# Kernel tuning notes

Hardware: AMD Instinct MI355X
Metric: run time of the kernel (lower is better)

## Reference

```python
import jax, jax.numpy as jnp
import numpy as np

SCALE = 8.0  # sqrt(hid=64), passed as init arg `scale`


def setup_inputs() -> dict:
    key = jax.random.key(0)
    kq, kk, kv, km = jax.random.split(key, 4)
    B, S, H = 32, 2048, 64  # B = bs*n_head
    q = jax.random.normal(kq, (B, S, H), dtype=jnp.float32)
    k = jax.random.normal(kk, (B, S, H), dtype=jnp.float32)
    v = jax.random.normal(kv, (B, S, H), dtype=jnp.float32)
    mask = jax.random.bernoulli(km, 0.1, (B, S, S))  # True = masked out
    return {"q": q, "k": k, "v": v, "mask": mask, "cca": 0}


def reference(q, k, v, mask, cca):
    # scores: [B, Sq, Sk]
    attn = jnp.einsum('bqh,bkh->bqk', q, k) / SCALE
    if mask is not None:
        attn = jnp.where(mask, jnp.finfo(q.dtype).min, attn)
    if cca:
        # CCA branch: softmax over the query/sequence axis (dim=1)
        attn = jax.nn.softmax(attn, axis=1)
        ctx = jnp.einsum('bq,bkh->bqh', attn.squeeze(-1)[..., None].squeeze(-1), v) if attn.ndim == 2 else jnp.einsum('bqk,bkh->bqh', attn, v)
    else:
        attn = jax.nn.softmax(attn, axis=2)
        ctx = jnp.einsum('bqk,bkh->bqh', attn, v)  # [B, Sq, H]
    return (ctx, attn)
```

## Files before the change

### kernel.cpp

```cpp
#include <hip/hip_runtime.h>
#include <hip/hip_bf16.h>

typedef __bf16  bf16x8_t __attribute__((ext_vector_type(8)));
typedef float   f32x4_t  __attribute__((ext_vector_type(4)));
typedef short   s16x8_t  __attribute__((ext_vector_type(8)));

#define S_LEN    2048
#define HDIM     64
#define BQ       16
#define NTHREADS 512
#define PSTR     2056
#define QSTR     72

__device__ __forceinline__ short f2bf(float f) {
    return __builtin_bit_cast(short, (__bf16)f);
}
__device__ __forceinline__ float bf2f(short s) {
    return __builtin_bit_cast(float, ((unsigned)(unsigned short)s) << 16);
}

__global__ void detect_mask(const unsigned char* __restrict__ M, int* __restrict__ flags) {
    __shared__ int cnt[4];
    if (threadIdx.x < 4) cnt[threadIdx.x] = 0;
    __syncthreads();
    int local[4] = {0, 0, 0, 0};
    for (int i = threadIdx.x; i < 16384; i += 256)
        if (M[i]) local[i & 3]++;
    #pragma unroll
    for (int c = 0; c < 4; ++c)
        if (local[c]) atomicAdd(&cnt[c], local[c]);
    __syncthreads();
    if (threadIdx.x == 0) {
        int stride;
        if (cnt[1] == 0 && cnt[2] == 0 && cnt[3] == 0)      stride = 4;
        else if (cnt[0] == 0 && cnt[1] == 0)                stride = 4;
        else                                                stride = 1;
        flags[0] = stride;
    }
}

__global__ __launch_bounds__(NTHREADS, 4)
void sdpa_fused(const float* __restrict__ Q, const float* __restrict__ K,
                const float* __restrict__ V, const unsigned char* __restrict__ M,
                const int* __restrict__ MF, float* __restrict__ OUT)
{
    __shared__ short Plds[BQ * PSTR];
    __shared__ short Qlds[BQ * QSTR];
    __shared__ float rowsum[BQ];

    const int tid  = threadIdx.x;
    const int wave = tid >> 6;
    const int lane = tid & 63;
    const int col  = lane & 15;
    const int kg   = lane >> 4;

    const int mstride = MF[0];

    const int id   = blockIdx.x;
    const int slot = id >> 3;
    const int b    = ((slot >> 7) << 3) | (id & 7);
    const int q0   = (slot & 127) * BQ;

    float* ctx_out  = OUT;
    float* attn_out = OUT + (size_t)32 * S_LEN * HDIM;

    {
        const int r  = tid >> 5;
        const int h2 = (tid & 31) * 2;
        const float2 qv = *(const float2*)(Q + ((size_t)b * S_LEN + q0 + r) * HDIM + h2);
        Qlds[r * QSTR + h2]     = f2bf(qv.x);
        Qlds[r * QSTR + h2 + 1] = f2bf(qv.y);
    }
    __syncthreads();

    bf16x8_t afrag[2];
    #pragma unroll
    for (int kk = 0; kk < 2; ++kk)
        afrag[kk] = *(const bf16x8_t*)&Qlds[col * QSTR + kk * 32 + kg * 8];

    {
        const float* Kb = K + (size_t)b * S_LEN * HDIM;
        #pragma unroll 2
        for (int f = 0; f < 16; ++f) {
            const int n0 = wave * 256 + f * 16;
            const float* kp = Kb + (n0 + col) * HDIM + kg * 8;
            const float4 ka = *(const float4*)kp;
            const float4 kb = *(const float4*)(kp + 4);
            const float4 kc = *(const float4*)(kp + 32);
            const float4 kd = *(const float4*)(kp + 36);
            s16x8_t b0s, b1s;
            b0s[0]=f2bf(ka.x); b0s[1]=f2bf(ka.y); b0s[2]=f2bf(ka.z); b0s[3]=f2bf(ka.w);
            b0s[4]=f2bf(kb.x); b0s[5]=f2bf(kb.y); b0s[6]=f2bf(kb.z); b0s[7]=f2bf(kb.w);
            b1s[0]=f2bf(kc.x); b1s[1]=f2bf(kc.y); b1s[2]=f2bf(kc.z); b1s[3]=f2bf(kc.w);
            b1s[4]=f2bf(kd.x); b1s[5]=f2bf(kd.y); b1s[6]=f2bf(kd.z); b1s[7]=f2bf(kd.w);
            f32x4_t acc = {0.f, 0.f, 0.f, 0.f};
            acc = __builtin_amdgcn_mfma_f32_16x16x32_bf16(afrag[0], __builtin_bit_cast(bf16x8_t, b0s), acc, 0, 0, 0);
            acc = __builtin_amdgcn_mfma_f32_16x16x32_bf16(afrag[1], __builtin_bit_cast(bf16x8_t, b1s), acc, 0, 0, 0);
            #pragma unroll
            for (int r = 0; r < 4; ++r)
                Plds[(kg*4 + r) * PSTR + n0 + col] = f2bf(__expf(acc[r] * 0.125f));
        }
    }
    __syncthreads();

    {
        const int row = tid >> 5;
        const int lr  = tid & 31;
        float s = 0.f;
        if (mstride == 1) {
            const unsigned char* mrow = M + (size_t)b * S_LEN * S_LEN + (size_t)(q0 + row) * S_LEN;
            #pragma unroll 2
            for (int i = 0; i < 8; ++i) {
                const int c0 = (lr + 32 * i) * 8;
                s16x8_t pv = *(s16x8_t*)&Plds[row * PSTR + c0];
                const uint2 mm = *(const uint2*)(mrow + c0);
                #pragma unroll
                for (int e = 0; e < 4; ++e) {
                    if ((mm.x >> (8*e)) & 0xFFu) pv[e] = 0; else s += bf2f(pv[e]);
                    if ((mm.y >> (8*e)) & 0xFFu) pv[4+e] = 0; else s += bf2f(pv[4+e]);
                }
                *(s16x8_t*)&Plds[row * PSTR + c0] = pv;
            }
        } else {
            const unsigned* mrow = (const unsigned*)M + (size_t)b * S_LEN * S_LEN + (size_t)(q0 + row) * S_LEN;
            #pragma unroll 2
            for (int i = 0; i < 8; ++i) {
                const int c0 = (lr + 32 * i) * 8;
                s16x8_t pv = *(s16x8_t*)&Plds[row * PSTR + c0];
                const uint4 w0 = *(const uint4*)(mrow + c0);
                const uint4 w1 = *(const uint4*)(mrow + c0 + 4);
                if (w0.x) pv[0] = 0; else s += bf2f(pv[0]);
                if (w0.y) pv[1] = 0; else s += bf2f(pv[1]);
                if (w0.z) pv[2] = 0; else s += bf2f(pv[2]);
                if (w0.w) pv[3] = 0; else s += bf2f(pv[3]);
                if (w1.x) pv[4] = 0; else s += bf2f(pv[4]);
                if (w1.y) pv[5] = 0; else s += bf2f(pv[5]);
                if (w1.z) pv[6] = 0; else s += bf2f(pv[6]);
                if (w1.w) pv[7] = 0; else s += bf2f(pv[7]);
                *(s16x8_t*)&Plds[row * PSTR + c0] = pv;
            }
        }
        s += __shfl_xor(s, 1);
        s += __shfl_xor(s, 2);
        s += __shfl_xor(s, 4);
        s += __shfl_xor(s, 8);
        s += __shfl_xor(s, 16);
        if (lr == 0) rowsum[row] = s;
    }
    __syncthreads();

    if (wave < 4) {
        float* ab = attn_out + ((size_t)b * S_LEN + q0) * S_LEN;
        #pragma unroll 2
        for (int it = 0; it < 16; ++it) {
            const int flat = it * 256 + tid;
            const int row  = flat >> 8;
            const int c0   = (flat & 255) * 8;
            const float inv = 1.0f / rowsum[row];
            const s16x8_t pv = *(const s16x8_t*)&Plds[row * PSTR + c0];
            float4 o0, o1;
            o0.x = bf2f(pv[0]) * inv; o0.y = bf2f(pv[1]) * inv;
            o0.z = bf2f(pv[2]) * inv; o0.w = bf2f(pv[3]) * inv;
            o1.x = bf2f(pv[4]) * inv; o1.y = bf2f(pv[5]) * inv;
            o1.z = bf2f(pv[6]) * inv; o1.w = bf2f(pv[7]) * inv;
            float* op = ab + (size_t)row * S_LEN + c0;
            *(float4*)op       = o0;
            *(float4*)(op + 4) = o1;
        }
    } else {
        const int hbase = (wave - 4) * 16;
        const float* Vb = V + (size_t)b * S_LEN * HDIM + hbase + col;

        float p0[8], p1[8];
        #define LOADV(k0, dst)                                          \
            { const float* vp = Vb + (size_t)((k0) + kg * 8) * HDIM;    \
              dst[0] = vp[0*HDIM]; dst[1] = vp[1*HDIM];                 \
              dst[2] = vp[2*HDIM]; dst[3] = vp[3*HDIM];                 \
              dst[4] = vp[4*HDIM]; dst[5] = vp[5*HDIM];                 \
              dst[6] = vp[6*HDIM]; dst[7] = vp[7*HDIM]; }
        #define PACK(src, dst)                                          \
            { s16x8_t t;                                                \
              t[0]=f2bf(src[0]); t[1]=f2bf(src[1]); t[2]=f2bf(src[2]);  \
              t[3]=f2bf(src[3]); t[4]=f2bf(src[4]); t[5]=f2bf(src[5]);  \
              t[6]=f2bf(src[6]); t[7]=f2bf(src[7]);                     \
              dst = __builtin_bit_cast(bf16x8_t, t); }

        LOADV(0,  p0);
        LOADV(32, p1);
        f32x4_t cacc = {0.f, 0.f, 0.f, 0.f};
        for (int kc2 = 0; kc2 < 32; ++kc2) {
            const int ke = kc2 * 2;
            {
                const bf16x8_t pa = *(const bf16x8_t*)&Plds[col * PSTR + ke*32 + kg*8];
                bf16x8_t vbf; PACK(p0, vbf);
                if (ke + 2 < 64) LOADV((ke + 2) * 32, p0);
                cacc = __builtin_amdgcn_mfma_f32_16x16x32_bf16(pa, vbf, cacc, 0, 0, 0);
            }
            {
                const bf16x8_t pa = *(const bf16x8_t*)&Plds[col * PSTR + (ke+1)*32 + kg*8];
                bf16x8_t vbf; PACK(p1, vbf);
                if (ke + 3 < 64) LOADV((ke + 3) * 32, p1);
                cacc = __builtin_amdgcn_mfma_f32_16x16x32_bf16(pa, vbf, cacc, 0, 0, 0);
            }
        }
        #undef LOADV
        #undef PACK
        #pragma unroll
        for (int r = 0; r < 4; ++r) {
            const int row = kg * 4 + r;
            ctx_out[((size_t)b * S_LEN + q0 + row) * HDIM + hbase + col] = cacc[r] / rowsum[row];
        }
    }
}

extern "C" void kernel_launch(void* const* d_in, const int* in_sizes, int n_in,
                              void* d_out, int out_size, void* d_ws, size_t ws_size,
                              hipStream_t stream)
{
    const float* q = (const float*)d_in[0];
    const float* k = (const float*)d_in[1];
    const float* v = (const float*)d_in[2];
    const unsigned char* mask = (const unsigned char*)d_in[3];
    int* mflags = (int*)d_ws;
    float* out = (float*)d_out;
    detect_mask<<<dim3(1), dim3(256), 0, stream>>>(mask, mflags);
    sdpa_fused<<<dim3(4096), dim3(NTHREADS), 0, stream>>>(q, k, v, mask, mflags, out);
}
```

Before: 508.2 us.

## Prefetch mask as bitmask, fuse masking into QK, split PV across all waves

The mask row block is loaded up front with nontemporal loads and compressed into a per-row bitmask in shared memory. Masking and row-sum accumulation are then folded into the QK^T/exp loop, which removes a separate pass over P and a barrier. The PV product is split across all eight waves by key halves, with a shared-memory reduction, and all waves now cooperate on the attention store using nontemporal stores. Extra shared memory (bitmask, partials) and more registers from the unrolled K prefetch could lower occupancy.

```diff
diff --git a/kernel.cpp b/kernel.cpp
--- a/kernel.cpp
+++ b/kernel.cpp
@@ -1,9 +1,10 @@
 #include <hip/hip_runtime.h>
 #include <hip/hip_bf16.h>
 
-typedef __bf16  bf16x8_t __attribute__((ext_vector_type(8)));
-typedef float   f32x4_t  __attribute__((ext_vector_type(4)));
-typedef short   s16x8_t  __attribute__((ext_vector_type(8)));
+typedef __bf16    bf16x8_t __attribute__((ext_vector_type(8)));
+typedef float     f32x4_t  __attribute__((ext_vector_type(4)));
+typedef short     s16x8_t  __attribute__((ext_vector_type(8)));
+typedef unsigned  u32x4_t  __attribute__((ext_vector_type(4)));
 
 #define S_LEN    2048
 #define HDIM     64
@@ -11,6 +12,7 @@
 #define NTHREADS 512
 #define PSTR     2056
 #define QSTR     72
+#define BMSTR    264
 
 __device__ __forceinline__ short f2bf(float f) {
     return __builtin_bit_cast(short, (__bf16)f);
@@ -46,14 +48,16 @@
 {
     __shared__ short Plds[BQ * PSTR];
     __shared__ short Qlds[BQ * QSTR];
+    __shared__ unsigned char Bm[BQ * BMSTR];
+    __shared__ float Pvp[4][BQ][17];
     __shared__ float rowsum[BQ];
+    __shared__ float rinv[BQ];
 
     const int tid  = threadIdx.x;
     const int wave = tid >> 6;
     const int lane = tid & 63;
     const int col  = lane & 15;
     const int kg   = lane >> 4;
-
     const int mstride = MF[0];
 
     const int id   = blockIdx.x;
@@ -70,6 +74,46 @@
         const float2 qv = *(const float2*)(Q + ((size_t)b * S_LEN + q0 + r) * HDIM + h2);
         Qlds[r * QSTR + h2]     = f2bf(qv.x);
         Qlds[r * QSTR + h2 + 1] = f2bf(qv.y);
+        if (tid < BQ) rowsum[tid] = 0.f;
+    }
+    {
+        const int row = tid >> 5;
+        const int seg = (tid & 31) * 64;
+        unsigned nib[16];
+        if (mstride == 1) {
+            const unsigned char* mp = M + (size_t)b * S_LEN * S_LEN
+                                        + (size_t)(q0 + row) * S_LEN + seg;
+            const u32x4_t m0 = __builtin_nontemporal_load((const u32x4_t*)(mp));
+            const u32x4_t m1 = __builtin_nontemporal_load((const u32x4_t*)(mp + 16));
+            const u32x4_t m2 = __builtin_nontemporal_load((const u32x4_t*)(mp + 32));
+            const u32x4_t m3 = __builtin_nontemporal_load((const u32x4_t*)(mp + 48));
+            const unsigned w[16] = {m0[0],m0[1],m0[2],m0[3], m1[0],m1[1],m1[2],m1[3],
+                                    m2[0],m2[1],m2[2],m2[3], m3[0],m3[1],m3[2],m3[3]};
+            #pragma unroll
+            for (int i = 0; i < 16; ++i) {
+                const unsigned t = (w[i] & 0x7F7F7F7Fu) + 0x7F7F7F7Fu;
+                const unsigned z = ((t | w[i]) & 0x80808080u) >> 7;
+                nib[i] = (z * 0x10204081u) >> 28;
+            }
+        } else {
+            const unsigned* mp = (const unsigned*)M + (size_t)b * S_LEN * S_LEN
+                                    + (size_t)(q0 + row) * S_LEN + seg;
+            #pragma unroll
+            for (int j = 0; j < 16; ++j) {
+                const u32x4_t wv = __builtin_nontemporal_load((const u32x4_t*)(mp + j * 4));
+                unsigned n = 0, t;
+                t = (wv[0] & 0x7FFFFFFFu) + 0x7FFFFFFFu; n |=  ((t | wv[0]) >> 31) & 1u;
+                t = (wv[1] & 0x7FFFFFFFu) + 0x7FFFFFFFu; n |= (((t | wv[1]) >> 31) & 1u) << 1;
+                t = (wv[2] & 0x7FFFFFFFu) + 0x7FFFFFFFu; n |= (((t | wv[2]) >> 31) & 1u) << 2;
+                t = (wv[3] & 0x7FFFFFFFu) + 0x7FFFFFFFu; n |= (((t | wv[3]) >> 31) & 1u) << 3;
+                nib[j] = n;
+            }
+        }
+        unsigned lo = 0, hi = 0;
+        #pragma unroll
+        for (int j = 0; j < 8; ++j) { lo |= nib[j] << (4 * j); hi |= nib[8 + j] << (4 * j); }
+        *(unsigned long long*)&Bm[row * BMSTR + (seg >> 3)] =
+            ((unsigned long long)hi << 32) | lo;
     }
     __syncthreads();
 
@@ -78,137 +122,126 @@
     for (int kk = 0; kk < 2; ++kk)
         afrag[kk] = *(const bf16x8_t*)&Qlds[col * QSTR + kk * 32 + kg * 8];
 
+    float rs[4] = {0.f, 0.f, 0.f, 0.f};
     {
         const float* Kb = K + (size_t)b * S_LEN * HDIM;
-        #pragma unroll 2
-        for (int f = 0; f < 16; ++f) {
-            const int n0 = wave * 256 + f * 16;
-            const float* kp = Kb + (n0 + col) * HDIM + kg * 8;
-            const float4 ka = *(const float4*)kp;
-            const float4 kb = *(const float4*)(kp + 4);
-            const float4 kc = *(const float4*)(kp + 32);
-            const float4 kd = *(const float4*)(kp + 36);
-            s16x8_t b0s, b1s;
-            b0s[0]=f2bf(ka.x); b0s[1]=f2bf(ka.y); b0s[2]=f2bf(ka.z); b0s[3]=f2bf(ka.w);
-            b0s[4]=f2bf(kb.x); b0s[5]=f2bf(kb.y); b0s[6]=f2bf(kb.z); b0s[7]=f2bf(kb.w);
-            b1s[0]=f2bf(kc.x); b1s[1]=f2bf(kc.y); b1s[2]=f2bf(kc.z); b1s[3]=f2bf(kc.w);
-            b1s[4]=f2bf(kd.x); b1s[5]=f2bf(kd.y); b1s[6]=f2bf(kd.z); b1s[7]=f2bf(kd.w);
-            f32x4_t acc = {0.f, 0.f, 0.f, 0.f};
-            acc = __builtin_amdgcn_mfma_f32_16x16x32_bf16(afrag[0], __builtin_bit_cast(bf16x8_t, b0s), acc, 0, 0, 0);
-            acc = __builtin_amdgcn_mfma_f32_16x16x32_bf16(afrag[1], __builtin_bit_cast(bf16x8_t, b1s), acc, 0, 0, 0);
-            #pragma unroll
-            for (int r = 0; r < 4; ++r)
-                Plds[(kg*4 + r) * PSTR + n0 + col] = f2bf(__expf(acc[r] * 0.125f));
-        }
-    }
-    __syncthreads();
-
-    {
-        const int row = tid >> 5;
-        const int lr  = tid & 31;
-        float s = 0.f;
-        if (mstride == 1) {
-            const unsigned char* mrow = M + (size_t)b * S_LEN * S_LEN + (size_t)(q0 + row) * S_LEN;
-            #pragma unroll 2
-            for (int i = 0; i < 8; ++i) {
-                const int c0 = (lr + 32 * i) * 8;
-                s16x8_t pv = *(s16x8_t*)&Plds[row * PSTR + c0];
-                const uint2 mm = *(const uint2*)(mrow + c0);
-                #pragma unroll
-                for (int e = 0; e < 4; ++e) {
-                    if ((mm.x >> (8*e)) & 0xFFu) pv[e] = 0; else s += bf2f(pv[e]);
-                    if ((mm.y >> (8*e)) & 0xFFu) pv[4+e] = 0; else s += bf2f(pv[4+e]);
-                }
-                *(s16x8_t*)&Plds[row * PSTR + c0] = pv;
-            }
-        } else {
-            const unsigned* mrow = (const unsigned*)M + (size_t)b * S_LEN * S_LEN + (size_t)(q0 + row) * S_LEN;
-            #pragma unroll 2
-            for (int i = 0; i < 8; ++i) {
-                const int c0 = (lr + 32 * i) * 8;
-                s16x8_t pv = *(s16x8_t*)&Plds[row * PSTR + c0];
-                const uint4 w0 = *(const uint4*)(mrow + c0);
-                const uint4 w1 = *(const uint4*)(mrow + c0 + 4);
-                if (w0.x) pv[0] = 0; else s += bf2f(pv[0]);
-                if (w0.y) pv[1] = 0; else s += bf2f(pv[1]);
-                if (w0.z) pv[2] = 0; else s += bf2f(pv[2]);
-                if (w0.w) pv[3] = 0; else s += bf2f(pv[3]);
-                if (w1.x) pv[4] = 0; else s += bf2f(pv[4]);
-                if (w1.y) pv[5] = 0; else s += bf2f(pv[5]);
-                if (w1.z) pv[6] = 0; else s += bf2f(pv[6]);
-                if (w1.w) pv[7] = 0; else s += bf2f(pv[7]);
-                *(s16x8_t*)&Plds[row * PSTR + c0] = pv;
-            }
-        }
+        float4 A0,B0,C0,D0, A1,B1,C1,D1;
+
+        #define LDK(f, Ax,Bx,Cx,Dx) { \
+            const float* kp = Kb + (size_t)(wave*256 + (f)*16 + col) * HDIM + kg*8; \
+            Ax = *(const float4*)kp;       Bx = *(const float4*)(kp + 4); \
+            Cx = *(const float4*)(kp + 32); Dx = *(const float4*)(kp + 36); }
+
+        #define STEP(f, Ax,Bx,Cx,Dx, PF, fpf) { \
+            s16x8_t t0, t1; \
+            t0[0]=f2bf(Ax.x); t0[1]=f2bf(Ax.y); t0[2]=f2bf(Ax.z); t0[3]=f2bf(Ax.w); \
+            t0[4]=f2bf(Bx.x); t0[5]=f2bf(Bx.y); t0[6]=f2bf(Bx.z); t0[7]=f2bf(Bx.w); \
+            t1[0]=f2bf(Cx.x); t1[1]=f2bf(Cx.y); t1[2]=f2bf(Cx.z); t1[3]=f2bf(Cx.w); \
+            t1[4]=f2bf(Dx.x); t1[5]=f2bf(Dx.y); t1[6]=f2bf(Dx.z); t1[7]=f2bf(Dx.w); \
+            if (PF) LDK(fpf, Ax,Bx,Cx,Dx); \
+            f32x4_t acc = {0.f,0.f,0.f,0.f}; \
+            acc = __builtin_amdgcn_mfma_f32_16x16x32_bf16(afrag[0], __builtin_bit_cast(bf16x8_t, t0), acc, 0,0,0); \
+            acc = __builtin_amdgcn_mfma_f32_16x16x32_bf16(afrag[1], __builtin_bit_cast(bf16x8_t, t1), acc, 0,0,0); \
+            const int c = wave*256 + (f)*16 + col; \
+            _Pragma("unroll") \
+            for (int r = 0; r < 4; ++r) { \
+                const int row = kg*4 + r; \
+                const unsigned bm = Bm[row * BMSTR + (c >> 3)]; \
+                const float p = __expf(acc[r] * 0.125f); \
+                const short pb = ((bm >> (col & 7)) & 1u) ? (short)0 : f2bf(p); \
+                rs[r] += bf2f(pb); \
+                Plds[row * PSTR + c] = pb; \
+            } }
+
+        LDK(0, A0,B0,C0,D0);
+        LDK(1, A1,B1,C1,D1);
+        #pragma unroll
+        for (int ff = 0; ff < 16; ff += 2) {
+            STEP(ff,     A0,B0,C0,D0, (ff + 2 < 16), ff + 2);
+            STEP(ff + 1, A1,B1,C1,D1, (ff + 3 < 16), ff + 3);
+        }
+        #undef LDK
+        #undef STEP
+    }
+    #pragma unroll
+    for (int r = 0; r < 4; ++r) {
+        float s = rs[r];
         s += __shfl_xor(s, 1);
         s += __shfl_xor(s, 2);
         s += __shfl_xor(s, 4);
         s += __shfl_xor(s, 8);
-        s += __shfl_xor(s, 16);
-        if (lr == 0) rowsum[row] = s;
+        if (col == 0) atomicAdd(&rowsum[kg * 4 + r], s);
+    }
+    __syncthreads();
+    if (tid < BQ) rinv[tid] = 1.0f / rowsum[tid];
+
+    const int hbase = (wave & 3) * 16;
+    const int kbase = (wave >> 2) * 1024;
+    f32x4_t cacc = {0.f, 0.f, 0.f, 0.f};
+    {
+        const float* Vb = V + (size_t)b * S_LEN * HDIM + hbase + col;
+        float vr0[8], vr1[8];
+        #define LOADV(k0, dst) { const float* vp = Vb + (size_t)((k0) + kg*8) * HDIM; \
+            dst[0]=vp[0*HDIM]; dst[1]=vp[1*HDIM]; dst[2]=vp[2*HDIM]; dst[3]=vp[3*HDIM]; \
+            dst[4]=vp[4*HDIM]; dst[5]=vp[5*HDIM]; dst[6]=vp[6*HDIM]; dst[7]=vp[7*HDIM]; }
+        #define PACKV(src, dst) { s16x8_t t; \
+            t[0]=f2bf(src[0]); t[1]=f2bf(src[1]); t[2]=f2bf(src[2]); t[3]=f2bf(src[3]); \
+            t[4]=f2bf(src[4]); t[5]=f2bf(src[5]); t[6]=f2bf(src[6]); t[7]=f2bf(src[7]); \
+            dst = __builtin_bit_cast(bf16x8_t, t); }
+        LOADV(kbase,      vr0);
+        LOADV(kbase + 32, vr1);
+        #pragma unroll
+        for (int kc2 = 0; kc2 < 16; ++kc2) {
+            const int ke = kbase + kc2 * 64;
+            {
+                const bf16x8_t pa = *(const bf16x8_t*)&Plds[col * PSTR + ke + kg * 8];
+                bf16x8_t vbf; PACKV(vr0, vbf);
+                if (kc2 < 15) LOADV(ke + 64, vr0);
+                cacc = __builtin_amdgcn_mfma_f32_16x16x32_bf16(pa, vbf, cacc, 0, 0, 0);
+            }
+            {
+                const bf16x8_t pa = *(const bf16x8_t*)&Plds[col * PSTR + ke + 32 + kg * 8];
+                bf16x8_t vbf; PACKV(vr1, vbf);
+                if (kc2 < 15) LOADV(ke + 96, vr1);
+                cacc = __builtin_amdgcn_mfma_f32_16x16x32_bf16(pa, vbf, cacc, 0, 0, 0);
+            }
+        }
+        #undef LOADV
+        #undef PACKV
+    }
+    if (wave >= 4) {
+        #pragma unroll
+        for (int r = 0; r < 4; ++r)
+            Pvp[wave - 4][kg * 4 + r][col] = cacc[r];
     }
     __syncthreads();
 
     if (wave < 4) {
+        #pragma unroll
+        for (int r = 0; r < 4; ++r) {
+            const int row = kg * 4 + r;
+            const float cv = (cacc[r] + Pvp[wave][row][col]) * rinv[row];
+            __builtin_nontemporal_store(cv,
+                ctx_out + ((size_t)b * S_LEN + q0 + row) * HDIM + hbase + col);
+        }
+    }
+    {
         float* ab = attn_out + ((size_t)b * S_LEN + q0) * S_LEN;
         #pragma unroll 2
-        for (int it = 0; it < 16; ++it) {
-            const int flat = it * 256 + tid;
+        for (int it = 0; it < 8; ++it) {
+            const int flat = it * 512 + tid;
             const int row  = flat >> 8;
             const int c0   = (flat & 255) * 8;
-            const float inv = 1.0f / rowsum[row];
+            const float inv = rinv[row];
             const s16x8_t pv = *(const s16x8_t*)&Plds[row * PSTR + c0];
-            float4 o0, o1;
-            o0.x = bf2f(pv[0]) * inv; o0.y = bf2f(pv[1]) * inv;
-            o0.z = bf2f(pv[2]) * inv; o0.w = bf2f(pv[3]) * inv;
-            o1.x = bf2f(pv[4]) * inv; o1.y = bf2f(pv[5]) * inv;
-            o1.z = bf2f(pv[6]) * inv; o1.w = bf2f(pv[7]) * inv;
+            f32x4_t o0, o1;
+            o0[0] = bf2f(pv[0]) * inv; o0[1] = bf2f(pv[1]) * inv;
+            o0[2] = bf2f(pv[2]) * inv; o0[3] = bf2f(pv[3]) * inv;
+            o1[0] = bf2f(pv[4]) * inv; o1[1] = bf2f(pv[5]) * inv;
+            o1[2] = bf2f(pv[6]) * inv; o1[3] = bf2f(pv[7]) * inv;
             float* op = ab + (size_t)row * S_LEN + c0;
-            *(float4*)op       = o0;
-            *(float4*)(op + 4) = o1;
-        }
-    } else {
-        const int hbase = (wave - 4) * 16;
-        const float* Vb = V + (size_t)b * S_LEN * HDIM + hbase + col;
-
-        float p0[8], p1[8];
-        #define LOADV(k0, dst)                                          \
-            { const float* vp = Vb + (size_t)((k0) + kg * 8) * HDIM;    \
-              dst[0] = vp[0*HDIM]; dst[1] = vp[1*HDIM];                 \
-              dst[2] = vp[2*HDIM]; dst[3] = vp[3*HDIM];                 \
-              dst[4] = vp[4*HDIM]; dst[5] = vp[5*HDIM];                 \
-              dst[6] = vp[6*HDIM]; dst[7] = vp[7*HDIM]; }
-        #define PACK(src, dst)                                          \
-            { s16x8_t t;                                                \
-              t[0]=f2bf(src[0]); t[1]=f2bf(src[1]); t[2]=f2bf(src[2]);  \
-              t[3]=f2bf(src[3]); t[4]=f2bf(src[4]); t[5]=f2bf(src[5]);  \
-              t[6]=f2bf(src[6]); t[7]=f2bf(src[7]);                     \
-              dst = __builtin_bit_cast(bf16x8_t, t); }
-
-        LOADV(0,  p0);
-        LOADV(32, p1);
-        f32x4_t cacc = {0.f, 0.f, 0.f, 0.f};
-        for (int kc2 = 0; kc2 < 32; ++kc2) {
-            const int ke = kc2 * 2;
-            {
-                const bf16x8_t pa = *(const bf16x8_t*)&Plds[col * PSTR + ke*32 + kg*8];
-                bf16x8_t vbf; PACK(p0, vbf);
-                if (ke + 2 < 64) LOADV((ke + 2) * 32, p0);
-                cacc = __builtin_amdgcn_mfma_f32_16x16x32_bf16(pa, vbf, cacc, 0, 0, 0);
-            }
-            {
-                const bf16x8_t pa = *(const bf16x8_t*)&Plds[col * PSTR + (ke+1)*32 + kg*8];
-                bf16x8_t vbf; PACK(p1, vbf);
-                if (ke + 3 < 64) LOADV((ke + 3) * 32, p1);
-                cacc = __builtin_amdgcn_mfma_f32_16x16x32_bf16(pa, vbf, cacc, 0, 0, 0);
-            }
-        }
-        #undef LOADV
-        #undef PACK
-        #pragma unroll
-        for (int r = 0; r < 4; ++r) {
-            const int row = kg * 4 + r;
-            ctx_out[((size_t)b * S_LEN + q0 + row) * HDIM + hbase + col] = cacc[r] / rowsum[row];
+            __builtin_nontemporal_store(o0, (f32x4_t*)op);
+            __builtin_nontemporal_store(o1, (f32x4_t*)(op + 4));
         }
     }
 }
```

After: 645.2 us. 1.27x slower.
